# Kernel tuning notes

Measured on AMD Instinct MI355X. Metric: run time of the kernel, lower is better.

The kernel has to match this reference:

```python
import jax, jax.numpy as jnp
import numpy as np

N = 10000      # nodes
E = 80000      # edges
D = 128        # d_model
H = 8          # num_heads
DH = 128       # d_head
DFF = 512      # d_ff
CLAMP = 5.0
EPS = 1e-5


def setup_inputs() -> dict:
    key = jax.random.key(0)
    ks = jax.random.split(key, 10)
    s = 0.05
    return {
        "feat": jax.random.normal(ks[0], (N, D), jnp.float32),
        "src": jax.random.randint(ks[1], (E,), 0, N),
        "dst": jax.random.randint(ks[2], (E,), 0, N),
        # projections stored as (in, out); x @ W == torch Linear(bias=False)
        "Wq": jax.random.normal(ks[3], (D, H * DH), jnp.float32) * s,
        "Wk": jax.random.normal(ks[4], (D, H * DH), jnp.float32) * s,
        "Wv": jax.random.normal(ks[5], (D, H * DH), jnp.float32) * s,
        "Wo": jax.random.normal(ks[6], (H * DH, D), jnp.float32) * s,
        "g1": jnp.ones((D,), jnp.float32),
        "b1": jnp.zeros((D,), jnp.float32),
        "W1": jax.random.normal(ks[7], (D, DFF), jnp.float32) * s,
        "bf1": jnp.zeros((DFF,), jnp.float32),
        "W2": jax.random.normal(ks[8], (DFF, D), jnp.float32) * s,
        "bf2": jnp.zeros((D,), jnp.float32),
        "g2": jnp.ones((D,), jnp.float32),
        "b2": jnp.zeros((D,), jnp.float32),
    }


def _layer_norm(x, g, b):
    mu = x.mean(-1, keepdims=True)
    xc = x - mu
    var = (xc * xc).mean(-1, keepdims=True)
    return xc * jax.lax.rsqrt(var + EPS) * g + b


def reference(feat, src, dst, Wq, Wk, Wv, Wo, g1, b1, W1, bf1, W2, bf2, g2, b2):
    h_src = feat[src]                              # (E, D) gather
    h_dst = feat[dst]                              # (E, D)
    q = (h_dst @ Wq).reshape(E, H, DH)             # query from destination node
    k = (h_src @ Wk).reshape(E, H, DH)
    v = (h_src @ Wv).reshape(E, H, DH)
    # per-edge logits: QK dot per head, scale, clamp
    u = jnp.clip((q * k).sum(-1) / np.sqrt(DH), -CLAMP, CLAMP)  # (E, H)
    # edge_softmax over incoming edges of each destination node
    m = jax.ops.segment_max(u, dst, num_segments=N)             # (N, H)
    ex = jnp.exp(u - m[dst])
    den = jax.ops.segment_sum(ex, dst, num_segments=N)          # (N, H)
    a = ex / den[dst]                                           # (E, H)
    # weighted V, segment-sum to destination nodes
    agg = jax.ops.segment_sum(a[..., None] * v, dst, num_segments=N)  # (N, H, DH)
    uh = _layer_norm(feat + agg.reshape(N, H * DH) @ Wo, g1, b1)
    ffn = jax.nn.relu(uh @ W1 + bf1) @ W2 + bf2
    return _layer_norm(uh + ffn, g2, b2)
```

## Files before the change

kernel.cpp:

```cpp
#include <hip/hip_runtime.h>

typedef unsigned int uint;
typedef unsigned short ushort;
typedef __attribute__((ext_vector_type(8))) short short8;
typedef __attribute__((ext_vector_type(4))) float f32x4;

#define DEV static __device__ __forceinline__

DEV float bf_lo(uint v) { return __uint_as_float(v << 16); }
DEV float bf_hi(uint v) { return __uint_as_float(v & 0xffff0000u); }
DEV ushort f2bf(float f) {
    uint u = __float_as_uint(f);
    u += 0x7fffu + ((u >> 16) & 1u);
    return (ushort)(u >> 16);
}
DEV void stC(float* p, float v) { *p = v; }
DEV void stC(ushort* p, float v) { *p = f2bf(v); }

#define DPPADD(v, ctrl) \
    ((v) + __int_as_float(__builtin_amdgcn_mov_dpp(__float_as_int(v), (ctrl), 0xF, 0xF, true)))

__global__ __launch_bounds__(256) void zero_kernel(int4* __restrict__ p, int n4)
{
    int i = blockIdx.x * 256 + threadIdx.x;
    if (i < n4) p[i] = int4{0, 0, 0, 0};
}

template <typename OT>
DEV void transp_body(float (*tile)[65], const float* __restrict__ in,
                     OT* __restrict__ out, int R, int C, int bid, int t)
{
    const int nbx = C >> 6;
    const int bx = bid % nbx, by = bid / nbx;
#pragma unroll
    for (int it = 0; it < 4; ++it) {
        int idx = it * 256 + t;
        int rr = idx >> 4, cc4 = (idx & 15) * 4;
        float4 v = *reinterpret_cast<const float4*>(in + (size_t)(by * 64 + rr) * C + bx * 64 + cc4);
        tile[cc4][rr] = v.x; tile[cc4 + 1][rr] = v.y;
        tile[cc4 + 2][rr] = v.z; tile[cc4 + 3][rr] = v.w;
    }
    __syncthreads();
#pragma unroll
    for (int it = 0; it < 4; ++it) {
        int idx = it * 256 + t;
        int cc = idx >> 4, rr4 = (idx & 15) * 4;
        OT* po = out + (size_t)(bx * 64 + cc) * R + by * 64 + rr4;
        if constexpr (__is_same(OT, float)) {
            float4 o = { tile[cc][rr4], tile[cc][rr4 + 1], tile[cc][rr4 + 2], tile[cc][rr4 + 3] };
            *reinterpret_cast<float4*>(po) = o;
        } else {
            ushort4 o = { f2bf(tile[cc][rr4]), f2bf(tile[cc][rr4 + 1]),
                          f2bf(tile[cc][rr4 + 2]), f2bf(tile[cc][rr4 + 3]) };
            *reinterpret_cast<ushort4*>(po) = o;
        }
    }
}

__global__ __launch_bounds__(256) void prep0_kernel(
    const float* __restrict__ feat, ushort* __restrict__ featbf,
    const float* __restrict__ Wo, float* __restrict__ WoT,
    const float* __restrict__ W1, ushort* __restrict__ W1T,
    const float* __restrict__ W2, ushort* __restrict__ W2T,
    const int* __restrict__ dst, int* __restrict__ cntd, int N, int E)
{
    __shared__ float tile[64][65];
    const int nf = (N * 32 + 255) / 256;
    const int b = blockIdx.x, t = threadIdx.x;
    if (b < nf) {
        int i = b * 256 + t;
        if (i >= N * 32) return;
        float4 v = reinterpret_cast<const float4*>(feat)[i];
        ushort4 o;
        o.x = f2bf(v.x); o.y = f2bf(v.y); o.z = f2bf(v.z); o.w = f2bf(v.w);
        reinterpret_cast<ushort4*>(featbf)[i] = o;
    } else if (b < nf + 32) {
        transp_body<float>(tile, Wo, WoT, 1024, 128, b - nf, t);
    } else if (b < nf + 48) {
        transp_body<ushort>(tile, W1, W1T, 128, 512, b - nf - 32, t);
    } else if (b < nf + 64) {
        transp_body<ushort>(tile, W2, W2T, 512, 128, b - nf - 48, t);
    } else {
        int e = (b - nf - 64) * 256 + t;
        if (e >= E) return;
        atomicAdd(&cntd[dst[e]], 1);
    }
}

__global__ __launch_bounds__(256) void mpt_mfma_kernel(
    const float* __restrict__ Wq, const float* __restrict__ Wk,
    const float* __restrict__ Wv, const float* __restrict__ WoT,
    ushort* __restrict__ MPT)
{
    __shared__ char lds[65536];
    char* As = lds;
    char* Bs = lds + 32768;

    const int part = blockIdx.x >> 3, h = blockIdx.x & 7;
    const int t = threadIdx.x;
    const int lane = t & 63, w = t >> 6;
    const int frow = lane & 15, kgrp = lane >> 4;

    const float* Asrc = part ? WoT : Wk;
    const float* Bsrc = part ? Wv : Wq;
    const float ascale = part ? 1.f : 0.08838834764831845f;

#pragma unroll
    for (int it = 0; it < 16; ++it) {
        int idx = it * 256 + t;
        int r = idx >> 5, c4 = (idx & 31) * 4;
        size_t goff = (size_t)r * 1024 + h * 128 + c4;
        float4 va = *reinterpret_cast<const float4*>(Asrc + goff);
        ushort4 ua = { f2bf(va.x * ascale), f2bf(va.y * ascale),
                       f2bf(va.z * ascale), f2bf(va.w * ascale) };
        *reinterpret_cast<ushort4*>(&As[r * 256 + ((c4 * 2) ^ ((r & 7) << 4))]) = ua;
        float4 vb = *reinterpret_cast<const float4*>(Bsrc + goff);
        ushort4 ub = { f2bf(vb.x), f2bf(vb.y), f2bf(vb.z), f2bf(vb.w) };
        *reinterpret_cast<ushort4*>(&Bs[r * 256 + ((c4 * 2) ^ ((r & 7) << 4))]) = ub;
    }
    __syncthreads();

    f32x4 acc[2][8] = {};
#pragma unroll
    for (int ks = 0; ks < 4; ++ks) {
        int koff = ks * 64 + kgrp * 16;
        short8 b[8];
#pragma unroll
        for (int fn = 0; fn < 8; ++fn) {
            int col = fn * 16 + frow;
            b[fn] = *reinterpret_cast<const short8*>(&Bs[col * 256 + (koff ^ ((col & 7) << 4))]);
        }
#pragma unroll
        for (int fm = 0; fm < 2; ++fm) {
            int row = w * 32 + fm * 16 + frow;
            short8 a = *reinterpret_cast<const short8*>(&As[row * 256 + (koff ^ ((row & 7) << 4))]);
#pragma unroll
            for (int fn = 0; fn < 8; ++fn)
                acc[fm][fn] = __builtin_amdgcn_mfma_f32_16x16x32_bf16(a, b[fn], acc[fm][fn], 0, 0, 0);
        }
    }

    const size_t base = ((size_t)part * 1024 + h * 128) * 128;
#pragma unroll
    for (int fm = 0; fm < 2; ++fm)
#pragma unroll
        for (int fn = 0; fn < 8; ++fn)
#pragma unroll
            for (int r = 0; r < 4; ++r) {
                int j = w * 32 + fm * 16 + kgrp * 4 + r;
                int i = fn * 16 + frow;
                MPT[base + (size_t)j * 128 + i] = f2bf(acc[fm][fn][r]);
            }
}

__global__ __launch_bounds__(1024) void scan1_kernel(
    const int* __restrict__ cntd, int* __restrict__ offd, int* __restrict__ curd, int N)
{
    __shared__ int ls[1024];
    const int t = threadIdx.x;
    const int chunk = (N + 1023) >> 10;
    int base = t * chunk;
    int s = 0;
    for (int i = 0; i < chunk; ++i) {
        int idx = base + i;
        if (idx < N) s += cntd[idx];
    }
    ls[t] = s;
    __syncthreads();
    for (int d = 1; d < 1024; d <<= 1) {
        int v = (t >= d) ? ls[t - d] : 0;
        __syncthreads();
        ls[t] += v;
        __syncthreads();
    }
    int run = t ? ls[t - 1] : 0;
    for (int i = 0; i < chunk; ++i) {
        int idx = base + i;
        if (idx < N) {
            offd[idx] = run;
            curd[idx] = run;
            run += cntd[idx];
        }
    }
    if (t == 1023) offd[N] = run;
}

__global__ void scat_kernel(const int* __restrict__ src, const int* __restrict__ dst,
                            int* __restrict__ curd,
                            int* __restrict__ src_d, int* __restrict__ dst_d, int E)
{
    int e = blockIdx.x * 256 + threadIdx.x;
    if (e >= E) return;
    int s = src[e], d = dst[e];
    int pd = atomicAdd(&curd[d], 1);
    src_d[pd] = s;
    dst_d[pd] = d;
}

template <int NTILE, typename OT, bool BIAS, bool RELU, bool RES>
__global__ __launch_bounds__(256) void gemm_mfma(
    const ushort* __restrict__ A, const ushort* __restrict__ BT,
    const float* __restrict__ bias, const float* __restrict__ res,
    OT* __restrict__ C, int M, int K, int NC)
{
    constexpr int FN = NTILE * 2;
    constexpr int WN = NTILE * 32;
    __shared__ char lds[16384 + NTILE * 8192];
    char* AsB = lds;
    char* BsB = lds + 16384;

    const int m0 = blockIdx.y * 128;
    const int n0 = blockIdx.x * (NTILE * 64);
    const int t = threadIdx.x;
    const int lane = t & 63, wid = t >> 6;
    const int wm = wid >> 1, wn = wid & 1;
    const int frow = lane & 15, kgrp = lane >> 4;

    f32x4 acc[4][FN] = {};

    for (int kk = 0; kk < K; kk += 64) {
#pragma unroll
        for (int it = 0; it < 4; ++it) {
            int q = it * 256 + t;
            int r = q >> 3, c8 = (q & 7) * 8;
            int gm = m0 + r;
            short8 v = {};
            if (gm < M) v = *reinterpret_cast<const short8*>(&A[(size_t)gm * K + kk + c8]);
            *reinterpret_cast<short8*>(&AsB[r * 128 + ((c8 * 2) ^ ((r & 7) << 4))]) = v;
        }
#pragma unroll
        for (int it = 0; it < 2 * NTILE; ++it) {
            int q = it * 256 + t;
            int r = q >> 3, c8 = (q & 7) * 8;
            short8 v = *reinterpret_cast<const short8*>(&BT[(size_t)(n0 + r) * K + kk + c8]);
            *reinterpret_cast<short8*>(&BsB[r * 128 + ((c8 * 2) ^ ((r & 7) << 4))]) = v;
        }
        __syncthreads();
#pragma unroll
        for (int kp = 0; kp < 2; ++kp) {
            const int koffb = kp * 64 + kgrp * 16;
            short8 b[FN];
#pragma unroll
            for (int fn = 0; fn < FN; ++fn) {
                int col = wn * WN + fn * 16 + frow;
                b[fn] = *reinterpret_cast<const short8*>(&BsB[col * 128 + (koffb ^ ((col & 7) << 4))]);
            }
#pragma unroll
            for (int fm = 0; fm < 4; ++fm) {
                int row = wm * 64 + fm * 16 + frow;
                short8 a = *reinterpret_cast<const short8*>(&AsB[row * 128 + (koffb ^ ((row & 7) << 4))]);
#pragma unroll
                for (int fn = 0; fn < FN; ++fn)
                    acc[fm][fn] = __builtin_amdgcn_mfma_f32_16x16x32_bf16(a, b[fn], acc[fm][fn], 0, 0, 0);
            }
        }
        __syncthreads();
    }

#pragma unroll
    for (int fm = 0; fm < 4; ++fm)
#pragma unroll
        for (int fn = 0; fn < FN; ++fn)
#pragma unroll
            for (int r = 0; r < 4; ++r) {
                int gm = m0 + wm * 64 + fm * 16 + kgrp * 4 + r;
                int gn = n0 + wn * WN + fn * 16 + frow;
                if (gm >= M) continue;
                float v = acc[fm][fn][r];
                if (BIAS) v += bias[gn];
                if (RELU) v = fmaxf(v, 0.f);
                if (RES) v += res[(size_t)gm * NC + gn];
                stC(&C[(size_t)gm * NC + gn], v);
            }
}

__global__ __launch_bounds__(256) void edge_logits2_kernel(
    const ushort* __restrict__ featbf, const ushort* __restrict__ GVO,
    const int* __restrict__ src_d, const int* __restrict__ dst_d,
    float* __restrict__ exws, int E)
{
    int w = (int)((blockIdx.x * 256 + threadIdx.x) >> 6);
    int lane = threadIdx.x & 63;
    int el = lane >> 4, li = lane & 15;
    int p = w * 4 + el;
    if (p >= E) return;
    int s = src_d[p], d = dst_d[p];
    uint4 f = reinterpret_cast<const uint4*>(featbf)[(size_t)s * 16 + li];
    const uint4* Grow = reinterpret_cast<const uint4*>(GVO) + (size_t)d * 256 + li;
    float sel = 0.f;
#pragma unroll
    for (int h = 0; h < 8; ++h) {
        uint4 g = Grow[h * 16];
        float pv = bf_lo(g.x) * bf_lo(f.x) + bf_hi(g.x) * bf_hi(f.x);
        pv += bf_lo(g.y) * bf_lo(f.y) + bf_hi(g.y) * bf_hi(f.y);
        pv += bf_lo(g.z) * bf_lo(f.z) + bf_hi(g.z) * bf_hi(f.z);
        pv += bf_lo(g.w) * bf_lo(f.w) + bf_hi(g.w) * bf_hi(f.w);
        pv = DPPADD(pv, 0xB1);
        pv = DPPADD(pv, 0x4E);
        pv = DPPADD(pv, 0x141);
        pv = DPPADD(pv, 0x128);
        sel = (li == h) ? pv : sel;
    }
    float u = fminf(fmaxf(sel, -5.f), 5.f);
    float ex = __expf(u);
    if (li < 8) exws[(size_t)p * 8 + li] = ex;
}

__global__ __launch_bounds__(256) void aggden_ln1_kernel(
    const ushort* __restrict__ GVO, const int* __restrict__ src_d,
    const int* __restrict__ offd, const float* __restrict__ exws,
    const float* __restrict__ feat, const float* __restrict__ g1,
    const float* __restrict__ b1, float* __restrict__ uh,
    ushort* __restrict__ uhbf, int N)
{
    int d = (int)((blockIdx.x * 256 + threadIdx.x) >> 6);
    int lane = threadIdx.x & 63;
    if (d >= N) return;
    const int lo = offd[d], hi = offd[d + 1];

    int h = lane & 7;
    float den = 0.f;
    for (int i = lo + (lane >> 3); i < hi; i += 8)
        den += exws[(size_t)i * 8 + h];
    den += __shfl_xor(den, 8);
    den += __shfl_xor(den, 16);
    den += __shfl_xor(den, 32);
    float rh = 1.f / den;
    float rv0 = __shfl(rh, 0), rv1 = __shfl(rh, 1), rv2 = __shfl(rh, 2), rv3 = __shfl(rh, 3);
    float rv4 = __shfl(rh, 4), rv5 = __shfl(rh, 5), rv6 = __shfl(rh, 6), rv7 = __shfl(rh, 7);

    float acc0 = 0.f, acc1 = 0.f;
    int snext = (lo < hi) ? src_d[lo] : 0;
    for (int i = lo; i < hi; ++i) {
        int s = snext;
        if (i + 1 < hi) snext = src_d[i + 1];
        float4 e0 = *reinterpret_cast<const float4*>(&exws[(size_t)i * 8]);
        float4 e1 = *reinterpret_cast<const float4*>(&exws[(size_t)i * 8 + 4]);
        const uint* vrow = reinterpret_cast<const uint*>(GVO + (size_t)s * 2048 + 1024);
        uint gv0 = vrow[0 * 64 + lane], gv1 = vrow[1 * 64 + lane];
        uint gv2 = vrow[2 * 64 + lane], gv3 = vrow[3 * 64 + lane];
        uint gv4 = vrow[4 * 64 + lane], gv5 = vrow[5 * 64 + lane];
        uint gv6 = vrow[6 * 64 + lane], gv7 = vrow[7 * 64 + lane];
        float a0 = e0.x * rv0, a1 = e0.y * rv1, a2 = e0.z * rv2, a3 = e0.w * rv3;
        float a4 = e1.x * rv4, a5 = e1.y * rv5, a6 = e1.z * rv6, a7 = e1.w * rv7;
        acc0 += a0 * bf_lo(gv0) + a1 * bf_lo(gv1) + a2 * bf_lo(gv2) + a3 * bf_lo(gv3)
              + a4 * bf_lo(gv4) + a5 * bf_lo(gv5) + a6 * bf_lo(gv6) + a7 * bf_lo(gv7);
        acc1 += a0 * bf_hi(gv0) + a1 * bf_hi(gv1) + a2 * bf_hi(gv2) + a3 * bf_hi(gv3)
              + a4 * bf_hi(gv4) + a5 * bf_hi(gv5) + a6 * bf_hi(gv6) + a7 * bf_hi(gv7);
    }

    float2 v = reinterpret_cast<const float2*>(feat)[(size_t)d * 64 + lane];
    v.x += acc0;
    v.y += acc1;
    float sum = v.x + v.y;
#pragma unroll
    for (int off = 32; off; off >>= 1) sum += __shfl_xor(sum, off);
    float mean = sum * (1.f / 128.f);
    float cx = v.x - mean, cy = v.y - mean;
    float vs = cx * cx + cy * cy;
#pragma unroll
    for (int off = 32; off; off >>= 1) vs += __shfl_xor(vs, off);
    float r = rsqrtf(vs * (1.f / 128.f) + 1e-5f);
    float2 gg = reinterpret_cast<const float2*>(g1)[lane];
    float2 bb = reinterpret_cast<const float2*>(b1)[lane];
    float2 o;
    o.x = cx * r * gg.x + bb.x;
    o.y = cy * r * gg.y + bb.y;
    reinterpret_cast<float2*>(uh)[(size_t)d * 64 + lane] = o;
    ushort2 ob; ob.x = f2bf(o.x); ob.y = f2bf(o.y);
    reinterpret_cast<ushort2*>(uhbf)[(size_t)d * 64 + lane] = ob;
}

__global__ __launch_bounds__(256) void ln_kernel(
    const float* __restrict__ x, const float* __restrict__ g,
    const float* __restrict__ b, float* __restrict__ out, int M)
{
    int row = (int)((blockIdx.x * 256 + threadIdx.x) >> 6);
    int lane = threadIdx.x & 63;
    if (row >= M) return;
    float2 v = reinterpret_cast<const float2*>(x)[(size_t)row * 64 + lane];
    float sum = v.x + v.y;
#pragma unroll
    for (int off = 32; off; off >>= 1) sum += __shfl_xor(sum, off);
    float mean = sum * (1.f / 128.f);
    float cx = v.x - mean, cy = v.y - mean;
    float vs = cx * cx + cy * cy;
#pragma unroll
    for (int off = 32; off; off >>= 1) vs += __shfl_xor(vs, off);
    float r = rsqrtf(vs * (1.f / 128.f) + 1e-5f);
    float2 gg = reinterpret_cast<const float2*>(g)[lane];
    float2 bb = reinterpret_cast<const float2*>(b)[lane];
    float2 o;
    o.x = cx * r * gg.x + bb.x;
    o.y = cy * r * gg.y + bb.y;
    reinterpret_cast<float2*>(out)[(size_t)row * 64 + lane] = o;
}

extern "C" void kernel_launch(void* const* d_in, const int* in_sizes, int n_in,
                              void* d_out, int out_size, void* d_ws, size_t ws_size,
                              hipStream_t stream)
{
    const float* feat = (const float*)d_in[0];
    const int*   src  = (const int*)d_in[1];
    const int*   dst  = (const int*)d_in[2];
    const float* Wq   = (const float*)d_in[3];
    const float* Wk   = (const float*)d_in[4];
    const float* Wv   = (const float*)d_in[5];
    const float* Wo   = (const float*)d_in[6];
    const float* g1   = (const float*)d_in[7];
    const float* b1   = (const float*)d_in[8];
    const float* W1   = (const float*)d_in[9];
    const float* bf1  = (const float*)d_in[10];
    const float* W2   = (const float*)d_in[11];
    const float* bf2  = (const float*)d_in[12];
    const float* g2   = (const float*)d_in[13];
    const float* b2   = (const float*)d_in[14];
    const int N = in_sizes[0] / 128;
    const int E = in_sizes[1];
    float* out = (float*)d_out;

    char* w = (char*)d_ws;
    auto alloc = [&](size_t bytes) {
        char* p = w;
        w += (bytes + 255) & ~(size_t)255;
        return p;
    };
    ushort* MPT    = (ushort*)alloc((size_t)2048 * 128 * 2);
    float*  WoT    = (float*)alloc((size_t)128 * 1024 * 4);
    ushort* W1T    = (ushort*)alloc((size_t)512 * 128 * 2);
    ushort* W2T    = (ushort*)alloc((size_t)128 * 512 * 2);
    ushort* featbf = (ushort*)alloc((size_t)N * 128 * 2);
    ushort* GVO    = (ushort*)alloc((size_t)N * 2048 * 2);
    float*  exws   = (float*)alloc((size_t)E * 8 * 4);
    int*    cntd   = (int*)alloc((size_t)((N + 3) & ~3) * 4);
    int*    offd   = (int*)alloc((size_t)(N + 1) * 4);
    int*    curd   = (int*)alloc((size_t)N * 4);
    int*    src_d  = (int*)alloc((size_t)E * 4);
    int*    dst_d  = (int*)alloc((size_t)E * 4);
    float*  uh     = (float*)alloc((size_t)N * 128 * 4);
    ushort* uhbf   = (ushort*)alloc((size_t)N * 128 * 2);
    ushort* f1     = (ushort*)alloc((size_t)N * 512 * 2);
    float*  pre2   = (float*)alloc((size_t)N * 128 * 4);

    int n4 = (N + 3) / 4;
    zero_kernel<<<(n4 + 255) / 256, 256, 0, stream>>>((int4*)cntd, n4);

    int nf = (N * 32 + 255) / 256;
    int eb = (E + 255) / 256;
    prep0_kernel<<<nf + 64 + eb, 256, 0, stream>>>(
        feat, featbf, Wo, WoT, W1, W1T, W2, W2T, dst, cntd, N, E);

    scan1_kernel<<<1, 1024, 0, stream>>>(cntd, offd, curd, N);
    scat_kernel<<<eb, 256, 0, stream>>>(src, dst, curd, src_d, dst_d, E);
    mpt_mfma_kernel<<<16, 256, 0, stream>>>(Wq, Wk, Wv, WoT, MPT);

    dim3 gv_grid(2048 / 128, (N + 127) / 128);
    gemm_mfma<2, ushort, false, false, false><<<gv_grid, 256, 0, stream>>>(
        featbf, MPT, nullptr, nullptr, GVO, N, 128, 2048);

    edge_logits2_kernel<<<(E + 15) / 16, 256, 0, stream>>>(featbf, GVO, src_d, dst_d, exws, E);
    int nwaves_n = (N * 64 + 255) / 256;
    aggden_ln1_kernel<<<nwaves_n, 256, 0, stream>>>(
        GVO, src_d, offd, exws, feat, g1, b1, uh, uhbf, N);

    dim3 f1_grid(512 / 128, (N + 127) / 128);
    gemm_mfma<2, ushort, true, true, false><<<f1_grid, 256, 0, stream>>>(
        uhbf, W1T, bf1, nullptr, f1, N, 128, 512);
    dim3 f2_grid(128 / 64, (N + 127) / 128);
    gemm_mfma<1, float, true, false, true><<<f2_grid, 256, 0, stream>>>(
        f1, W2T, bf2, uh, pre2, N, 512, 128);

    ln_kernel<<<nwaves_n, 256, 0, stream>>>(pre2, g2, b2, out, N);
}
```

Before: 139.9 us.

## Merge edge scatter with MPT GEMM launch and add single-pass K=128 GEMM

Edge scatter-by-destination and the fused weight-product MFMA kernel now run as one launch, with block index selecting the role, which removes one kernel launch and lets the two independent jobs overlap. A new gemm_k128 kernel loads the whole K=128 slab of A and B into LDS at once and does a single sync, with no K-loop. It replaces the general tiled GEMM for the GVO projection and the first FFN layer. The larger LDS footprint (64KB per block) may lower occupancy, and global loads are no longer overlapped with compute.

Measured after the change: 149.0 us. +6.6%, slower.

```diff
diff --git a/kernel.cpp b/kernel.cpp
--- a/kernel.cpp
+++ b/kernel.cpp
@@ -87,17 +87,61 @@
     }
 }
 
-__global__ __launch_bounds__(256) void mpt_mfma_kernel(
+__global__ __launch_bounds__(1024) void scan1_kernel(
+    const int* __restrict__ cntd, int* __restrict__ offd, int* __restrict__ curd, int N)
+{
+    __shared__ int ls[1024];
+    const int t = threadIdx.x;
+    const int chunk = (N + 1023) >> 10;
+    int base = t * chunk;
+    int s = 0;
+    for (int i = 0; i < chunk; ++i) {
+        int idx = base + i;
+        if (idx < N) s += cntd[idx];
+    }
+    ls[t] = s;
+    __syncthreads();
+    for (int d = 1; d < 1024; d <<= 1) {
+        int v = (t >= d) ? ls[t - d] : 0;
+        __syncthreads();
+        ls[t] += v;
+        __syncthreads();
+    }
+    int run = t ? ls[t - 1] : 0;
+    for (int i = 0; i < chunk; ++i) {
+        int idx = base + i;
+        if (idx < N) {
+            offd[idx] = run;
+            curd[idx] = run;
+            run += cntd[idx];
+        }
+    }
+    if (t == 1023) offd[N] = run;
+}
+
+__global__ __launch_bounds__(256) void scat_mpt_kernel(
+    const int* __restrict__ src, const int* __restrict__ dst,
+    int* __restrict__ curd, int* __restrict__ src_d, int* __restrict__ dst_d, int E, int eb,
     const float* __restrict__ Wq, const float* __restrict__ Wk,
     const float* __restrict__ Wv, const float* __restrict__ WoT,
     ushort* __restrict__ MPT)
 {
     __shared__ char lds[65536];
+    const int b = blockIdx.x, t = threadIdx.x;
+    if (b < eb) {
+        int e = b * 256 + t;
+        if (e >= E) return;
+        int s = src[e], d = dst[e];
+        int pd = atomicAdd(&curd[d], 1);
+        src_d[pd] = s;
+        dst_d[pd] = d;
+        return;
+    }
     char* As = lds;
     char* Bs = lds + 32768;
 
-    const int part = blockIdx.x >> 3, h = blockIdx.x & 7;
-    const int t = threadIdx.x;
+    const int mb = b - eb;
+    const int part = mb >> 3, h = mb & 7;
     const int lane = t & 63, w = t >> 6;
     const int frow = lane & 15, kgrp = lane >> 4;
 
@@ -124,11 +168,11 @@
 #pragma unroll
     for (int ks = 0; ks < 4; ++ks) {
         int koff = ks * 64 + kgrp * 16;
-        short8 b[8];
+        short8 bfr[8];
 #pragma unroll
         for (int fn = 0; fn < 8; ++fn) {
             int col = fn * 16 + frow;
-            b[fn] = *reinterpret_cast<const short8*>(&Bs[col * 256 + (koff ^ ((col & 7) << 4))]);
+            bfr[fn] = *reinterpret_cast<const short8*>(&Bs[col * 256 + (koff ^ ((col & 7) << 4))]);
         }
 #pragma unroll
         for (int fm = 0; fm < 2; ++fm) {
@@ -136,7 +180,7 @@
             short8 a = *reinterpret_cast<const short8*>(&As[row * 256 + (koff ^ ((row & 7) << 4))]);
 #pragma unroll
             for (int fn = 0; fn < 8; ++fn)
-                acc[fm][fn] = __builtin_amdgcn_mfma_f32_16x16x32_bf16(a, b[fn], acc[fm][fn], 0, 0, 0);
+                acc[fm][fn] = __builtin_amdgcn_mfma_f32_16x16x32_bf16(a, bfr[fn], acc[fm][fn], 0, 0, 0);
         }
     }
 
@@ -153,48 +197,77 @@
             }
 }
 
-__global__ __launch_bounds__(1024) void scan1_kernel(
-    const int* __restrict__ cntd, int* __restrict__ offd, int* __restrict__ curd, int N)
-{
-    __shared__ int ls[1024];
+template <int NTILE, typename OT, bool BIAS, bool RELU>
+__global__ __launch_bounds__(256) void gemm_k128(
+    const ushort* __restrict__ A, const ushort* __restrict__ BT,
+    const float* __restrict__ bias,
+    OT* __restrict__ C, int M, int NC)
+{
+    constexpr int FN = NTILE * 2;
+    constexpr int WN = NTILE * 32;
+    __shared__ char lds[32768 + NTILE * 16384];
+    char* AsB = lds;
+    char* BsB = lds + 32768;
+
+    const int m0 = blockIdx.y * 128;
+    const int n0 = blockIdx.x * (NTILE * 64);
     const int t = threadIdx.x;
-    const int chunk = (N + 1023) >> 10;
-    int base = t * chunk;
-    int s = 0;
-    for (int i = 0; i < chunk; ++i) {
-        int idx = base + i;
-        if (idx < N) s += cntd[idx];
-    }
-    ls[t] = s;
+    const int lane = t & 63, wid = t >> 6;
+    const int wm = wid >> 1, wn = wid & 1;
+    const int frow = lane & 15, kgrp = lane >> 4;
+
+#pragma unroll
+    for (int it = 0; it < 16; ++it) {
+        int q = it * 256 + t;
+        int r = q >> 4, c8 = (q & 15) * 8;
+        int gm = m0 + r;
+        short8 v = {};
+        if (gm < M) v = *reinterpret_cast<const short8*>(&A[(size_t)gm * 128 + c8]);
+        *reinterpret_cast<short8*>(&AsB[r * 256 + ((c8 * 2) ^ ((r & 7) << 4))]) = v;
+    }
+#pragma unroll
+    for (int it = 0; it < 8 * NTILE; ++it) {
+        int q = it * 256 + t;
+        int r = q >> 4, c8 = (q & 15) * 8;
+        short8 v = *reinterpret_cast<const short8*>(&BT[(size_t)(n0 + r) * 128 + c8]);
+        *reinterpret_cast<short8*>(&BsB[r * 256 + ((c8 * 2) ^ ((r & 7) << 4))]) = v;
+    }
     __syncthreads();
-    for (int d = 1; d < 1024; d <<= 1) {
-        int v = (t >= d) ? ls[t - d] : 0;
-        __syncthreads();
-        ls[t] += v;
-        __syncthreads();
-    }
-    int run = t ? ls[t - 1] : 0;
-    for (int i = 0; i < chunk; ++i) {
-        int idx = base + i;
-        if (idx < N) {
-            offd[idx] = run;
-            curd[idx] = run;
-            run += cntd[idx];
-        }
-    }
-    if (t == 1023) offd[N] = run;
-}
-
-__global__ void scat_kernel(const int* __restrict__ src, const int* __restrict__ dst,
-                            int* __restrict__ curd,
-                            int* __restrict__ src_d, int* __restrict__ dst_d, int E)
-{
-    int e = blockIdx.x * 256 + threadIdx.x;
-    if (e >= E) return;
-    int s = src[e], d = dst[e];
-    int pd = atomicAdd(&curd[d], 1);
-    src_d[pd] = s;
-    dst_d[pd] = d;
+
+    f32x4 acc[4][FN] = {};
+#pragma unroll
+    for (int kp = 0; kp < 4; ++kp) {
+        const int koff = kp * 64 + kgrp * 16;
+        short8 b[FN];
+#pragma unroll
+        for (int fn = 0; fn < FN; ++fn) {
+            int col = wn * WN + fn * 16 + frow;
+            b[fn] = *reinterpret_cast<const short8*>(&BsB[col * 256 + (koff ^ ((col & 7) << 4))]);
+        }
+#pragma unroll
+        for (int fm = 0; fm < 4; ++fm) {
+            int row = wm * 64 + fm * 16 + frow;
+            short8 a = *reinterpret_cast<const short8*>(&AsB[row * 256 + (koff ^ ((row & 7) << 4))]);
+#pragma unroll
+            for (int fn = 0; fn < FN; ++fn)
+                acc[fm][fn] = __builtin_amdgcn_mfma_f32_16x16x32_bf16(a, b[fn], acc[fm][fn], 0, 0, 0);
+        }
+    }
+
+#pragma unroll
+    for (int fm = 0; fm < 4; ++fm)
+#pragma unroll
+        for (int fn = 0; fn < FN; ++fn)
+#pragma unroll
+            for (int r = 0; r < 4; ++r) {
+                int gm = m0 + wm * 64 + fm * 16 + kgrp * 4 + r;
+                int gn = n0 + wn * WN + fn * 16 + frow;
+                if (gm >= M) continue;
+                float v = acc[fm][fn][r];
+                if (BIAS) v += bias[gn];
+                if (RELU) v = fmaxf(v, 0.f);
+                stC(&C[(size_t)gm * NC + gn], v);
+            }
 }
 
 template <int NTILE, typename OT, bool BIAS, bool RELU, bool RES>
@@ -451,12 +524,12 @@
         feat, featbf, Wo, WoT, W1, W1T, W2, W2T, dst, cntd, N, E);
 
     scan1_kernel<<<1, 1024, 0, stream>>>(cntd, offd, curd, N);
-    scat_kernel<<<eb, 256, 0, stream>>>(src, dst, curd, src_d, dst_d, E);
-    mpt_mfma_kernel<<<16, 256, 0, stream>>>(Wq, Wk, Wv, WoT, MPT);
+    scat_mpt_kernel<<<eb + 16, 256, 0, stream>>>(
+        src, dst, curd, src_d, dst_d, E, eb, Wq, Wk, Wv, WoT, MPT);
 
     dim3 gv_grid(2048 / 128, (N + 127) / 128);
-    gemm_mfma<2, ushort, false, false, false><<<gv_grid, 256, 0, stream>>>(
-        featbf, MPT, nullptr, nullptr, GVO, N, 128, 2048);
+    gemm_k128<2, ushort, false, false><<<gv_grid, 256, 0, stream>>>(
+        featbf, MPT, nullptr, GVO, N, 2048);
 
     edge_logits2_kernel<<<(E + 15) / 16, 256, 0, stream>>>(featbf, GVO, src_d, dst_d, exws, E);
     int nwaves_n = (N * 64 + 255) / 256;
@@ -464,8 +537,8 @@
         GVO, src_d, offd, exws, feat, g1, b1, uh, uhbf, N);
 
     dim3 f1_grid(512 / 128, (N + 127) / 128);
-    gemm_mfma<2, ushort, true, true, false><<<f1_grid, 256, 0, stream>>>(
-        uhbf, W1T, bf1, nullptr, f1, N, 128, 512);
+    gemm_k128<2, ushort, true, true><<<f1_grid, 256, 0, stream>>>(
+        uhbf, W1T, bf1, f1, N, 512);
     dim3 f2_grid(128 / 64, (N + 127) / 128);
     gemm_mfma<1, float, true, false, true><<<f2_grid, 256, 0, stream>>>(
         f1, W2T, bf2, uh, pre2, N, 512, 128);
```
